# Performance work log

Hardware: AMD Instinct MI355X
Metric: run time of the kernel (lower is better)

The kernel has to match this reference:

```python
import jax, jax.numpy as jnp
import numpy as np

N, NFEAT, NHID, NHEADS = 4096, 512, 64, 8
P = 65536
ALPHA = 0.2  # LeakyReLU negative slope
NEG = -9e15  # mask value used by standard dense GAT


def setup_inputs() -> dict:
    key = jax.random.key(0)
    ks = jax.random.split(key, 9)
    x = jax.random.normal(ks[0], (N, NFEAT), dtype=jnp.float32)
    adj = (jax.random.uniform(ks[1], (N, N)) < 0.01).astype(jnp.float32)  # sparse-ish binary graph
    s = 0.05
    W_heads = jax.random.normal(ks[2], (NHEADS, NFEAT, NHID), dtype=jnp.float32) * s
    a_heads = jax.random.normal(ks[3], (NHEADS, 2 * NHID), dtype=jnp.float32) * s
    W_out = jax.random.normal(ks[4], (NHID * NHEADS, NHID), dtype=jnp.float32) * s
    a_out = jax.random.normal(ks[5], (2 * NHID,), dtype=jnp.float32) * s
    W_score = jax.random.normal(ks[6], (NHID, NHID), dtype=jnp.float32) * s
    pair1_idx = jax.random.randint(ks[7], (P,), 0, N, dtype=jnp.int32)
    pair2_idx = jax.random.randint(ks[8], (P,), 0, N, dtype=jnp.int32)
    return dict(x=x, adj=adj, W_heads=W_heads, a_heads=a_heads,
                W_out=W_out, a_out=a_out, W_score=W_score,
                pair1_idx=pair1_idx, pair2_idx=pair2_idx)


def _gat_layer(h, adj, W, a, concat):
    # Standard dense GraphAttentionLayer (no dropout: eval mode)
    Wh = h @ W                       # [N, out]
    out = W.shape[1]
    e_src = Wh @ a[:out]             # [N]
    e_dst = Wh @ a[out:]             # [N]
    e = jax.nn.leaky_relu(e_src[:, None] + e_dst[None, :], ALPHA)  # [N, N]
    logits = jnp.where(adj > 0, e, NEG)
    attn = jax.nn.softmax(logits, axis=1)
    hp = attn @ Wh                   # [N, out]
    return jax.nn.elu(hp) if concat else hp


def reference(x, adj, W_heads, a_heads, W_out, a_out, W_score, pair1_idx, pair2_idx):
    # multi-head layer, vmapped over heads; each head: [N, NHID]
    heads = jax.vmap(lambda W, a: _gat_layer(x, adj, W, a, True))(W_heads, a_heads)
    h = jnp.transpose(heads, (1, 0, 2)).reshape(N, NHEADS * NHID)  # concat dim=1
    h = jax.nn.elu(_gat_layer(h, adj, W_out, a_out, False))        # [N, NHID]
    embed1 = h[pair1_idx]            # sparse.mm(pair1_map, h) == row gather
    embed2 = h[pair2_idx]
    # diag(embed1 @ W_score @ embed2.T) == rowwise dot
    scores = jnp.sum((embed1 @ W_score) * embed2, axis=1)  # [P]
    return scores
```

## Files before the change

### kernel.cpp

```cpp
#include <hip/hip_runtime.h>
#include <math.h>

#define N 4096
#define NFEAT 512
#define NHID 64
#define NHEADS 8
#define P_PAIRS 65536
#define CAP 128
#define LRELU_ALPHA 0.2f

typedef short bf16x8 __attribute__((ext_vector_type(8)));
typedef float f32x4 __attribute__((ext_vector_type(4)));

__device__ __forceinline__ unsigned short f2bf(float f) {
  unsigned u = __float_as_uint(f);
  u = u + 0x7FFFu + ((u >> 16) & 1u);
  return (unsigned short)(u >> 16);
}
__device__ __forceinline__ float bf2f(unsigned short h) {
  return __uint_as_float(((unsigned)h) << 16);
}

__device__ __forceinline__ int swz(int row, int s) {
  int sl = ((row & 7) * 32 + s) ^ ((row & 7) << 3);
  return (row >> 3) * 256 + sl;
}

__global__ __launch_bounds__(256) void prep_all(const float* __restrict__ adj,
                                                const float* __restrict__ W1,
                                                const float* __restrict__ W2,
                                                int* __restrict__ counts,
                                                int* __restrict__ cols,
                                                unsigned short* __restrict__ w1hi,
                                                unsigned short* __restrict__ w1lo,
                                                unsigned short* __restrict__ w2hi,
                                                unsigned short* __restrict__ w2lo,
                                                float* __restrict__ sum1,
                                                float* __restrict__ sum2) {
  int b = blockIdx.x;
  if (b < N) {
    if (b == 0) {
      for (int t = threadIdx.x; t < 512; t += 256) sum1[t] = 0.f;
      if (threadIdx.x < 64) sum2[threadIdx.x] = 0.f;
    }
    __shared__ int cnt;
    if (threadIdx.x == 0) cnt = 0;
    __syncthreads();
    const float4* arow = (const float4*)(adj + (size_t)b * N);
    for (int c4 = threadIdx.x; c4 < N / 4; c4 += 256) {
      float4 v = arow[c4];
      int base = c4 * 4;
      if (v.x > 0.f) { int k = atomicAdd(&cnt, 1); if (k < CAP) cols[(size_t)b * CAP + k] = base; }
      if (v.y > 0.f) { int k = atomicAdd(&cnt, 1); if (k < CAP) cols[(size_t)b * CAP + k] = base + 1; }
      if (v.z > 0.f) { int k = atomicAdd(&cnt, 1); if (k < CAP) cols[(size_t)b * CAP + k] = base + 2; }
      if (v.w > 0.f) { int k = atomicAdd(&cnt, 1); if (k < CAP) cols[(size_t)b * CAP + k] = base + 3; }
    }
    __syncthreads();
    if (threadIdx.x == 0) counts[b] = cnt < CAP ? cnt : CAP;
  } else {
    int c = b - N;
    const float* W;
    unsigned short *hiP, *loP;
    if (c < 512) { W = W1; hiP = w1hi; loP = w1lo; }
    else         { W = W2; hiP = w2hi; loP = w2lo; c -= 512; }
    const float* Wp = W + (size_t)(c >> 6) * 512 * 64 + (c & 63);
    for (int k = threadIdx.x; k < 512; k += 256) {
      float v = Wp[(size_t)k * 64];
      unsigned short hb = f2bf(v);
      hiP[(size_t)c * 512 + k] = hb;
      loP[(size_t)c * 512 + k] = f2bf(v - bf2f(hb));
    }
  }
}

template <bool F32A>
__global__ __launch_bounds__(512) void mfma_gemm(const float* __restrict__ Af,
                                                 const unsigned short* __restrict__ Ahi,
                                                 const unsigned short* __restrict__ Alo,
                                                 const unsigned short* __restrict__ Bhi,
                                                 const unsigned short* __restrict__ Blo,
                                                 const float* __restrict__ aVec,
                                                 float* __restrict__ C,
                                                 float* __restrict__ esrc,
                                                 float* __restrict__ edst,
                                                 float* __restrict__ sumAtomic) {
  __shared__ unsigned short As[2][2][128 * 32];
  __shared__ unsigned short Bs[2][2][64 * 32];
  const int t = threadIdx.x;
  const int m0 = blockIdx.x * 128;
  const int c0 = blockIdx.y * 64;
  const int lane = t & 63, wave = t >> 6;
  const int g = lane >> 4, r = lane & 15;
  const int wm = (wave >> 1) * 32;
  const int wn = (wave & 1) * 32;
  const int sar = t >> 2, sak = (t & 3) * 8;
  const int tb = t & 255;
  const int sbr = tb >> 2, sbk = (tb & 3) * 8;
  const unsigned short* Bsel = (t < 256) ? Bhi : Blo;
  const int bhalf = (t < 256) ? 0 : 1;
  const int idxA = swz(sar, sak);
  const int idxB = swz(sbr, sbk);
  const size_t aOff = (size_t)(m0 + sar) * 512 + sak;
  const size_t bOff = (size_t)(c0 + sbr) * 512 + sbk;
  const f32x4 z = {0.f, 0.f, 0.f, 0.f};
  f32x4 acc[2][2];
  acc[0][0] = z; acc[0][1] = z; acc[1][0] = z; acc[1][1] = z;

  int4 a0, a1, b0;
  auto loadRegs = [&](int kb) {
    if constexpr (F32A) {
      float4 v0 = *(const float4*)(Af + aOff + kb);
      float4 v1 = *(const float4*)(Af + aOff + kb + 4);
      unsigned h0 = f2bf(v0.x), h1 = f2bf(v0.y), h2 = f2bf(v0.z), h3 = f2bf(v0.w);
      unsigned h4 = f2bf(v1.x), h5 = f2bf(v1.y), h6 = f2bf(v1.z), h7 = f2bf(v1.w);
      unsigned l0 = f2bf(v0.x - bf2f(h0)), l1 = f2bf(v0.y - bf2f(h1));
      unsigned l2 = f2bf(v0.z - bf2f(h2)), l3 = f2bf(v0.w - bf2f(h3));
      unsigned l4 = f2bf(v1.x - bf2f(h4)), l5 = f2bf(v1.y - bf2f(h5));
      unsigned l6 = f2bf(v1.z - bf2f(h6)), l7 = f2bf(v1.w - bf2f(h7));
      a0.x = h0 | (h1 << 16); a0.y = h2 | (h3 << 16);
      a0.z = h4 | (h5 << 16); a0.w = h6 | (h7 << 16);
      a1.x = l0 | (l1 << 16); a1.y = l2 | (l3 << 16);
      a1.z = l4 | (l5 << 16); a1.w = l6 | (l7 << 16);
    } else {
      a0 = *(const int4*)(Ahi + aOff + kb);
      a1 = *(const int4*)(Alo + aOff + kb);
    }
    b0 = *(const int4*)(Bsel + bOff + kb);
  };
  auto storeLds = [&](int buf) {
    *(int4*)(&As[buf][0][idxA]) = a0;
    *(int4*)(&As[buf][1][idxA]) = a1;
    *(int4*)(&Bs[buf][bhalf][idxB]) = b0;
  };

  loadRegs(0);
  storeLds(0);
  __syncthreads();

  for (int ch = 0; ch < 16; ++ch) {
    const int cur = ch & 1;
    if (ch < 15) loadRegs((ch + 1) * 32);
    bf16x8 ah[2], al[2], bh[2], bl[2];
#pragma unroll
    for (int f = 0; f < 2; ++f) {
      int ia = swz(wm + f * 16 + r, 8 * g);
      int ib = swz(wn + f * 16 + r, 8 * g);
      ah[f] = *(const bf16x8*)(&As[cur][0][ia]);
      al[f] = *(const bf16x8*)(&As[cur][1][ia]);
      bh[f] = *(const bf16x8*)(&Bs[cur][0][ib]);
      bl[f] = *(const bf16x8*)(&Bs[cur][1][ib]);
    }
#pragma unroll
    for (int i = 0; i < 2; ++i)
#pragma unroll
      for (int j = 0; j < 2; ++j) {
        acc[i][j] = __builtin_amdgcn_mfma_f32_16x16x32_bf16(ah[i], bh[j], acc[i][j], 0, 0, 0);
        acc[i][j] = __builtin_amdgcn_mfma_f32_16x16x32_bf16(al[i], bh[j], acc[i][j], 0, 0, 0);
        acc[i][j] = __builtin_amdgcn_mfma_f32_16x16x32_bf16(ah[i], bl[j], acc[i][j], 0, 0, 0);
      }
    if (ch < 15) {
      storeLds(cur ^ 1);
      __syncthreads();
    }
  }

  __syncthreads();
  float* Cs = (float*)&As[0][0][0];
#pragma unroll
  for (int i = 0; i < 2; ++i)
#pragma unroll
    for (int j = 0; j < 2; ++j)
#pragma unroll
      for (int q = 0; q < 4; ++q)
        Cs[(wm + i * 16 + 4 * g + q) * 64 + wn + j * 16 + r] = acc[i][j][q];
  __syncthreads();
  float* Cp = C + ((size_t)blockIdx.y * N + m0) * 64;
  const float* aV = aVec + (size_t)blockIdx.y * 128;
  float as_ = aV[lane], ad_ = aV[64 + lane];
  float cs = 0.f;
#pragma unroll
  for (int rr = 0; rr < 16; ++rr) {
    int row = wave * 16 + rr;
    float v = Cs[row * 64 + lane];
    Cp[(size_t)row * 64 + lane] = v;
    cs += v;
    float s = v * as_, d = v * ad_;
#pragma unroll
    for (int off = 32; off; off >>= 1) {
      s += __shfl_xor(s, off);
      d += __shfl_xor(d, off);
    }
    if (lane == 0) {
      esrc[(size_t)blockIdx.y * N + m0 + row] = s;
      edst[(size_t)blockIdx.y * N + m0 + row] = d;
    }
  }
  atomicAdd(&sumAtomic[blockIdx.y * 64 + lane], cs);
}

__global__ __launch_bounds__(256) void gat_attn_l1(const float* __restrict__ Wh,
                                                   const float* __restrict__ esrc,
                                                   const float* __restrict__ edst,
                                                   const int* __restrict__ counts,
                                                   const int* __restrict__ cols,
                                                   const float* __restrict__ sumWh,
                                                   unsigned short* __restrict__ hhi,
                                                   unsigned short* __restrict__ hlo) {
  int h = blockIdx.x & 7;
  int wv = threadIdx.x >> 6;
  int lane = threadIdx.x & 63;
  int sg = lane >> 4, sl = lane & 15;
  int i = (blockIdx.x >> 3) * 4 + wv;
  int cnt = counts[i];
  __shared__ int jls[4][CAP];
  __shared__ float pls[4][CAP];
  const float* WhH = Wh + (size_t)h * N * 64;
  float4 acc = {0.f, 0.f, 0.f, 0.f};
  if (cnt == 0) {
    float4 sv = *(const float4*)(sumWh + h * 64 + 4 * sl);
    acc.x = sv.x * (1.0f / N); acc.y = sv.y * (1.0f / N);
    acc.z = sv.z * (1.0f / N); acc.w = sv.w * (1.0f / N);
  } else {
    const int* cl = cols + (size_t)i * CAP;
    jls[wv][lane] = (lane < cnt) ? cl[lane] : 0;
    jls[wv][lane + 64] = (lane + 64 < cnt) ? cl[lane + 64] : 0;
    float ei = esrc[h * N + i];
    const float* ed = edst + (size_t)h * N;
    float e0 = -1e30f, e1 = -1e30f;
    if (lane < cnt) {
      float e = ei + ed[jls[wv][lane]];
      e0 = (e > 0.f) ? e : LRELU_ALPHA * e;
    }
    if (lane + 64 < cnt) {
      float e = ei + ed[jls[wv][lane + 64]];
      e1 = (e > 0.f) ? e : LRELU_ALPHA * e;
    }
    float m = fmaxf(e0, e1);
#pragma unroll
    for (int off = 32; off; off >>= 1) m = fmaxf(m, __shfl_xor(m, off));
    float p0 = (lane < cnt) ? __expf(e0 - m) : 0.f;
    float p1 = (lane + 64 < cnt) ? __expf(e1 - m) : 0.f;
    float ssum = p0 + p1;
#pragma unroll
    for (int off = 32; off; off >>= 1) ssum += __shfl_xor(ssum, off);
    pls[wv][lane] = p0;
    pls[wv][lane + 64] = p1;
    int L = (cnt + 15) & ~15;
    for (int k = 0; k < L; k += 16) {
      int j0 = jls[wv][k + sg];
      int j1 = jls[wv][k + 4 + sg];
      int j2 = jls[wv][k + 8 + sg];
      int j3 = jls[wv][k + 12 + sg];
      float4 v0 = *(const float4*)(WhH + ((size_t)j0 << 6) + 4 * sl);
      float4 v1 = *(const float4*)(WhH + ((size_t)j1 << 6) + 4 * sl);
      float4 v2 = *(const float4*)(WhH + ((size_t)j2 << 6) + 4 * sl);
      float4 v3 = *(const float4*)(WhH + ((size_t)j3 << 6) + 4 * sl);
      float q0 = pls[wv][k + sg];
      float q1 = pls[wv][k + 4 + sg];
      float q2 = pls[wv][k + 8 + sg];
      float q3 = pls[wv][k + 12 + sg];
      acc.x = fmaf(q0, v0.x, acc.x); acc.y = fmaf(q0, v0.y, acc.y);
      acc.z = fmaf(q0, v0.z, acc.z); acc.w = fmaf(q0, v0.w, acc.w);
      acc.x = fmaf(q1, v1.x, acc.x); acc.y = fmaf(q1, v1.y, acc.y);
      acc.z = fmaf(q1, v1.z, acc.z); acc.w = fmaf(q1, v1.w, acc.w);
      acc.x = fmaf(q2, v2.x, acc.x); acc.y = fmaf(q2, v2.y, acc.y);
      acc.z = fmaf(q2, v2.z, acc.z); acc.w = fmaf(q2, v2.w, acc.w);
      acc.x = fmaf(q3, v3.x, acc.x); acc.y = fmaf(q3, v3.y, acc.y);
      acc.z = fmaf(q3, v3.z, acc.z); acc.w = fmaf(q3, v3.w, acc.w);
    }
    acc.x += __shfl_xor(acc.x, 16); acc.y += __shfl_xor(acc.y, 16);
    acc.z += __shfl_xor(acc.z, 16); acc.w += __shfl_xor(acc.w, 16);
    acc.x += __shfl_xor(acc.x, 32); acc.y += __shfl_xor(acc.y, 32);
    acc.z += __shfl_xor(acc.z, 32); acc.w += __shfl_xor(acc.w, 32);
    float inv = 1.0f / ssum;
    acc.x *= inv; acc.y *= inv; acc.z *= inv; acc.w *= inv;
  }
  if (sg == 0) {
    acc.x = (acc.x > 0.f) ? acc.x : expm1f(acc.x);
    acc.y = (acc.y > 0.f) ? acc.y : expm1f(acc.y);
    acc.z = (acc.z > 0.f) ? acc.z : expm1f(acc.z);
    acc.w = (acc.w > 0.f) ? acc.w : expm1f(acc.w);
    ushort4 hi4, lo4;
    hi4.x = f2bf(acc.x); lo4.x = f2bf(acc.x - bf2f(hi4.x));
    hi4.y = f2bf(acc.y); lo4.y = f2bf(acc.y - bf2f(hi4.y));
    hi4.z = f2bf(acc.z); lo4.z = f2bf(acc.z - bf2f(hi4.z));
    hi4.w = f2bf(acc.w); lo4.w = f2bf(acc.w - bf2f(hi4.w));
    size_t o = (size_t)i * 512 + h * 64 + 4 * sl;
    *(ushort4*)(hhi + o) = hi4;
    *(ushort4*)(hlo + o) = lo4;
  }
}

__global__ __launch_bounds__(256) void gat_attn_l2(const float* __restrict__ Wh,
                                                   const float* __restrict__ esrc,
                                                   const float* __restrict__ edst,
                                                   const int* __restrict__ counts,
                                                   const int* __restrict__ cols,
                                                   const float* __restrict__ sumWh,
                                                   const float* __restrict__ Wsc,
                                                   float* __restrict__ hf,
                                                   float* __restrict__ g) {
  __shared__ float Ws[64][64];
  int t = threadIdx.x;
#pragma unroll
  for (int j = 0; j < 4; ++j) {
    int q = t + j * 256;
    int k = q >> 4, cq = (q & 15) * 4;
    *(float4*)(&Ws[k][cq]) = *(const float4*)(Wsc + k * 64 + cq);
  }
  __syncthreads();
  int wv = t >> 6;
  int lane = t & 63;
  int sg = lane >> 4, sl = lane & 15;
  int i = (blockIdx.x << 2) + wv;
  int cnt = counts[i];
  __shared__ int jls[4][CAP];
  __shared__ float pls[4][CAP];
  float v;
  if (cnt == 0) {
    v = sumWh[lane] * (1.0f / N);
  } else {
    const int* cl = cols + (size_t)i * CAP;
    jls[wv][lane] = (lane < cnt) ? cl[lane] : 0;
    jls[wv][lane + 64] = (lane + 64 < cnt) ? cl[lane + 64] : 0;
    float ei = esrc[i];
    float e0 = -1e30f, e1 = -1e30f;
    if (lane < cnt) {
      float e = ei + edst[jls[wv][lane]];
      e0 = (e > 0.f) ? e : LRELU_ALPHA * e;
    }
    if (lane + 64 < cnt) {
      float e = ei + edst[jls[wv][lane + 64]];
      e1 = (e > 0.f) ? e : LRELU_ALPHA * e;
    }
    float m = fmaxf(e0, e1);
#pragma unroll
    for (int off = 32; off; off >>= 1) m = fmaxf(m, __shfl_xor(m, off));
    float p0 = (lane < cnt) ? __expf(e0 - m) : 0.f;
    float p1 = (lane + 64 < cnt) ? __expf(e1 - m) : 0.f;
    float ssum = p0 + p1;
#pragma unroll
    for (int off = 32; off; off >>= 1) ssum += __shfl_xor(ssum, off);
    pls[wv][lane] = p0;
    pls[wv][lane + 64] = p1;
    float4 acc = {0.f, 0.f, 0.f, 0.f};
    int L = (cnt + 15) & ~15;
    for (int k = 0; k < L; k += 16) {
      int j0 = jls[wv][k + sg];
      int j1 = jls[wv][k + 4 + sg];
      int j2 = jls[wv][k + 8 + sg];
      int j3 = jls[wv][k + 12 + sg];
      float4 v0 = *(const float4*)(Wh + ((size_t)j0 << 6) + 4 * sl);
      float4 v1 = *(const float4*)(Wh + ((size_t)j1 << 6) + 4 * sl);
      float4 v2 = *(const float4*)(Wh + ((size_t)j2 << 6) + 4 * sl);
      float4 v3 = *(const float4*)(Wh + ((size_t)j3 << 6) + 4 * sl);
      float q0 = pls[wv][k + sg];
      float q1 = pls[wv][k + 4 + sg];
      float q2 = pls[wv][k + 8 + sg];
      float q3 = pls[wv][k + 12 + sg];
      acc.x = fmaf(q0, v0.x, acc.x); acc.y = fmaf(q0, v0.y, acc.y);
      acc.z = fmaf(q0, v0.z, acc.z); acc.w = fmaf(q0, v0.w, acc.w);
      acc.x = fmaf(q1, v1.x, acc.x); acc.y = fmaf(q1, v1.y, acc.y);
      acc.z = fmaf(q1, v1.z, acc.z); acc.w = fmaf(q1, v1.w, acc.w);
      acc.x = fmaf(q2, v2.x, acc.x); acc.y = fmaf(q2, v2.y, acc.y);
      acc.z = fmaf(q2, v2.z, acc.z); acc.w = fmaf(q2, v2.w, acc.w);
      acc.x = fmaf(q3, v3.x, acc.x); acc.y = fmaf(q3, v3.y, acc.y);
      acc.z = fmaf(q3, v3.z, acc.z); acc.w = fmaf(q3, v3.w, acc.w);
    }
    acc.x += __shfl_xor(acc.x, 16); acc.y += __shfl_xor(acc.y, 16);
    acc.z += __shfl_xor(acc.z, 16); acc.w += __shfl_xor(acc.w, 16);
    acc.x += __shfl_xor(acc.x, 32); acc.y += __shfl_xor(acc.y, 32);
    acc.z += __shfl_xor(acc.z, 32); acc.w += __shfl_xor(acc.w, 32);
    float cx = __shfl(acc.x, lane >> 2);
    float cy = __shfl(acc.y, lane >> 2);
    float cz = __shfl(acc.z, lane >> 2);
    float cw = __shfl(acc.w, lane >> 2);
    int cmp = lane & 3;
    v = (cmp == 0) ? cx : (cmp == 1) ? cy : (cmp == 2) ? cz : cw;
    v /= ssum;
  }
  v = (v > 0.f) ? v : expm1f(v);
  hf[((size_t)i << 6) + lane] = v;
  float gacc = 0.f;
#pragma unroll
  for (int k = 0; k < 64; ++k)
    gacc = fmaf(__shfl(v, k), Ws[k][lane], gacc);
  g[((size_t)i << 6) + lane] = gacc;
}

__global__ __launch_bounds__(256) void score_quad(const float* __restrict__ g,
                                                  const float* __restrict__ hf,
                                                  const int* __restrict__ p1,
                                                  const int* __restrict__ p2,
                                                  float* __restrict__ out) {
  int w = threadIdx.x >> 6;
  int lane = threadIdx.x & 63;
  int sub = lane >> 4, sl = lane & 15;
  int p = (((blockIdx.x << 2) + w) << 2) + sub;
  int i1 = p1[p], i2 = p2[p];
  float4 ga = *(const float4*)(g + ((size_t)i1 << 6) + sl * 4);
  float4 hb = *(const float4*)(hf + ((size_t)i2 << 6) + sl * 4);
  float v = ga.x * hb.x + ga.y * hb.y + ga.z * hb.z + ga.w * hb.w;
#pragma unroll
  for (int off = 8; off; off >>= 1) v += __shfl_xor(v, off);
  if (sl == 0) out[p] = v;
}

extern "C" void kernel_launch(void* const* d_in, const int* in_sizes, int n_in,
                              void* d_out, int out_size, void* d_ws, size_t ws_size,
                              hipStream_t stream) {
  const float* x       = (const float*)d_in[0];
  const float* adj     = (const float*)d_in[1];
  const float* W_heads = (const float*)d_in[2];
  const float* a_heads = (const float*)d_in[3];
  const float* W_out   = (const float*)d_in[4];
  const float* a_out   = (const float*)d_in[5];
  const float* W_score = (const float*)d_in[6];
  const int* p1        = (const int*)d_in[7];
  const int* p2        = (const int*)d_in[8];
  float* out           = (float*)d_out;

  char* ws = (char*)d_ws;
  size_t off = 0;
  auto alloc = [&](size_t bytes) -> void* {
    void* p = ws + off;
    off += (bytes + 255) & ~(size_t)255;
    return p;
  };
  int*   counts = (int*)alloc((size_t)N * 4);
  int*   cols   = (int*)alloc((size_t)N * CAP * 4);
  unsigned short* wt1hi = (unsigned short*)alloc((size_t)512 * 512 * 2);
  unsigned short* wt1lo = (unsigned short*)alloc((size_t)512 * 512 * 2);
  unsigned short* wt2hi = (unsigned short*)alloc((size_t)64 * 512 * 2);
  unsigned short* wt2lo = (unsigned short*)alloc((size_t)64 * 512 * 2);
  float* Wh1    = (float*)alloc((size_t)NHEADS * N * 64 * 4);
  float* es1    = (float*)alloc((size_t)NHEADS * N * 4);
  float* ed1    = (float*)alloc((size_t)NHEADS * N * 4);
  float* sum1   = (float*)alloc((size_t)512 * 4);
  unsigned short* h1hi = (unsigned short*)alloc((size_t)N * 512 * 2);
  unsigned short* h1lo = (unsigned short*)alloc((size_t)N * 512 * 2);
  float* Wh2    = (float*)alloc((size_t)N * 64 * 4);
  float* es2    = (float*)alloc((size_t)N * 4);
  float* ed2    = (float*)alloc((size_t)N * 4);
  float* sum2   = (float*)alloc((size_t)64 * 4);
  float* hf     = (float*)alloc((size_t)N * 64 * 4);
  float* g      = (float*)alloc((size_t)N * 64 * 4);

  prep_all<<<N + 576, 256, 0, stream>>>(adj, W_heads, W_out, counts, cols,
                                        wt1hi, wt1lo, wt2hi, wt2lo, sum1, sum2);

  mfma_gemm<true><<<dim3(N / 128, NHEADS), 512, 0, stream>>>(
      x, nullptr, nullptr, wt1hi, wt1lo, a_heads, Wh1, es1, ed1, sum1);

  gat_attn_l1<<<(N / 4) * NHEADS, 256, 0, stream>>>(Wh1, es1, ed1, counts, cols,
                                                    sum1, h1hi, h1lo);

  mfma_gemm<false><<<dim3(N / 128, 1), 512, 0, stream>>>(
      nullptr, h1hi, h1lo, wt2hi, wt2lo, a_out, Wh2, es2, ed2, sum2);

  gat_attn_l2<<<N / 4, 256, 0, stream>>>(Wh2, es2, ed2, counts, cols, sum2,
                                         W_score, hf, g);

  score_quad<<<P_PAIRS / 16, 256, 0, stream>>>(g, hf, p1, p2, out);
}
```

Baseline: 102.0 us.

## Fuse adjacency scan into first GEMM launch and score pass into layer-2 tail

```diff
diff --git a/kernel.cpp b/kernel.cpp
--- a/kernel.cpp
+++ b/kernel.cpp
@@ -8,6 +8,8 @@
 #define P_PAIRS 65536
 #define CAP 128
 #define LRELU_ALPHA 0.2f
+#define GEMM_BLOCKS 256
+#define TAIL_BLOCKS 512
 
 typedef short bf16x8 __attribute__((ext_vector_type(8)));
 typedef float f32x4 __attribute__((ext_vector_type(4)));
@@ -26,69 +28,44 @@
   return (row >> 3) * 256 + sl;
 }
 
-__global__ __launch_bounds__(256) void prep_all(const float* __restrict__ adj,
-                                                const float* __restrict__ W1,
-                                                const float* __restrict__ W2,
-                                                int* __restrict__ counts,
-                                                int* __restrict__ cols,
-                                                unsigned short* __restrict__ w1hi,
-                                                unsigned short* __restrict__ w1lo,
-                                                unsigned short* __restrict__ w2hi,
-                                                unsigned short* __restrict__ w2lo,
-                                                float* __restrict__ sum1,
-                                                float* __restrict__ sum2) {
-  int b = blockIdx.x;
-  if (b < N) {
-    if (b == 0) {
-      for (int t = threadIdx.x; t < 512; t += 256) sum1[t] = 0.f;
-      if (threadIdx.x < 64) sum2[threadIdx.x] = 0.f;
-    }
-    __shared__ int cnt;
-    if (threadIdx.x == 0) cnt = 0;
-    __syncthreads();
-    const float4* arow = (const float4*)(adj + (size_t)b * N);
-    for (int c4 = threadIdx.x; c4 < N / 4; c4 += 256) {
-      float4 v = arow[c4];
-      int base = c4 * 4;
-      if (v.x > 0.f) { int k = atomicAdd(&cnt, 1); if (k < CAP) cols[(size_t)b * CAP + k] = base; }
-      if (v.y > 0.f) { int k = atomicAdd(&cnt, 1); if (k < CAP) cols[(size_t)b * CAP + k] = base + 1; }
-      if (v.z > 0.f) { int k = atomicAdd(&cnt, 1); if (k < CAP) cols[(size_t)b * CAP + k] = base + 2; }
-      if (v.w > 0.f) { int k = atomicAdd(&cnt, 1); if (k < CAP) cols[(size_t)b * CAP + k] = base + 3; }
-    }
-    __syncthreads();
-    if (threadIdx.x == 0) counts[b] = cnt < CAP ? cnt : CAP;
-  } else {
-    int c = b - N;
-    const float* W;
-    unsigned short *hiP, *loP;
-    if (c < 512) { W = W1; hiP = w1hi; loP = w1lo; }
-    else         { W = W2; hiP = w2hi; loP = w2lo; c -= 512; }
-    const float* Wp = W + (size_t)(c >> 6) * 512 * 64 + (c & 63);
-    for (int k = threadIdx.x; k < 512; k += 256) {
-      float v = Wp[(size_t)k * 64];
-      unsigned short hb = f2bf(v);
-      hiP[(size_t)c * 512 + k] = hb;
-      loP[(size_t)c * 512 + k] = f2bf(v - bf2f(hb));
-    }
+__global__ __launch_bounds__(256) void prep_wt(const float* __restrict__ W1,
+                                               const float* __restrict__ W2,
+                                               unsigned short* __restrict__ w1hi,
+                                               unsigned short* __restrict__ w1lo,
+                                               unsigned short* __restrict__ w2hi,
+                                               unsigned short* __restrict__ w2lo,
+                                               int* __restrict__ barrier) {
+  if (blockIdx.x == 0 && threadIdx.x == 0) *barrier = 0;
+  int c = blockIdx.x;
+  const float* W;
+  unsigned short *hiP, *loP;
+  if (c < 512) { W = W1; hiP = w1hi; loP = w1lo; }
+  else         { W = W2; hiP = w2hi; loP = w2lo; c -= 512; }
+  const float* Wp = W + (size_t)(c >> 6) * 512 * 64 + (c & 63);
+  for (int k = threadIdx.x; k < 512; k += 256) {
+    float v = Wp[(size_t)k * 64];
+    unsigned short hb = f2bf(v);
+    hiP[(size_t)c * 512 + k] = hb;
+    loP[(size_t)c * 512 + k] = f2bf(v - bf2f(hb));
   }
 }
 
 template <bool F32A>
-__global__ __launch_bounds__(512) void mfma_gemm(const float* __restrict__ Af,
-                                                 const unsigned short* __restrict__ Ahi,
-                                                 const unsigned short* __restrict__ Alo,
-                                                 const unsigned short* __restrict__ Bhi,
-                                                 const unsigned short* __restrict__ Blo,
-                                                 const float* __restrict__ aVec,
-                                                 float* __restrict__ C,
-                                                 float* __restrict__ esrc,
-                                                 float* __restrict__ edst,
-                                                 float* __restrict__ sumAtomic) {
-  __shared__ unsigned short As[2][2][128 * 32];
-  __shared__ unsigned short Bs[2][2][64 * 32];
+__device__ __forceinline__ void gemm_body(unsigned short* As, unsigned short* Bs,
+                                          int mIdx, int head,
+                                          const float* __restrict__ Af,
+                                          const unsigned short* __restrict__ Ahi,
+                                          const unsigned short* __restrict__ Alo,
+                                          const unsigned short* __restrict__ Bhi,
+                                          const unsigned short* __restrict__ Blo,
+                                          const float* __restrict__ aVec,
+                                          float* __restrict__ C,
+                                          float* __restrict__ esrc,
+                                          float* __restrict__ edst,
+                                          float* __restrict__ cpart) {
   const int t = threadIdx.x;
-  const int m0 = blockIdx.x * 128;
-  const int c0 = blockIdx.y * 64;
+  const int m0 = mIdx * 128;
+  const int c0 = head * 64;
   const int lane = t & 63, wave = t >> 6;
   const int g = lane >> 4, r = lane & 15;
   const int wm = (wave >> 1) * 32;
@@ -128,9 +105,9 @@
     b0 = *(const int4*)(Bsel + bOff + kb);
   };
   auto storeLds = [&](int buf) {
-    *(int4*)(&As[buf][0][idxA]) = a0;
-    *(int4*)(&As[buf][1][idxA]) = a1;
-    *(int4*)(&Bs[buf][bhalf][idxB]) = b0;
+    *(int4*)(&As[(buf * 2 + 0) * 4096 + idxA]) = a0;
+    *(int4*)(&As[(buf * 2 + 1) * 4096 + idxA]) = a1;
+    *(int4*)(&Bs[(buf * 2 + bhalf) * 2048 + idxB]) = b0;
   };
 
   loadRegs(0);
@@ -145,10 +122,10 @@
     for (int f = 0; f < 2; ++f) {
       int ia = swz(wm + f * 16 + r, 8 * g);
       int ib = swz(wn + f * 16 + r, 8 * g);
-      ah[f] = *(const bf16x8*)(&As[cur][0][ia]);
-      al[f] = *(const bf16x8*)(&As[cur][1][ia]);
-      bh[f] = *(const bf16x8*)(&Bs[cur][0][ib]);
-      bl[f] = *(const bf16x8*)(&Bs[cur][1][ib]);
+      ah[f] = *(const bf16x8*)(&As[(cur * 2 + 0) * 4096 + ia]);
+      al[f] = *(const bf16x8*)(&As[(cur * 2 + 1) * 4096 + ia]);
+      bh[f] = *(const bf16x8*)(&Bs[(cur * 2 + 0) * 2048 + ib]);
+      bl[f] = *(const bf16x8*)(&Bs[(cur * 2 + 1) * 2048 + ib]);
     }
 #pragma unroll
     for (int i = 0; i < 2; ++i)
@@ -165,7 +142,7 @@
   }
 
   __syncthreads();
-  float* Cs = (float*)&As[0][0][0];
+  float* Cs = (float*)As;
 #pragma unroll
   for (int i = 0; i < 2; ++i)
 #pragma unroll
@@ -174,8 +151,8 @@
       for (int q = 0; q < 4; ++q)
         Cs[(wm + i * 16 + 4 * g + q) * 64 + wn + j * 16 + r] = acc[i][j][q];
   __syncthreads();
-  float* Cp = C + ((size_t)blockIdx.y * N + m0) * 64;
-  const float* aV = aVec + (size_t)blockIdx.y * 128;
+  float* Cp = C + ((size_t)head * N + m0) * 64;
+  const float* aV = aVec + (size_t)head * 128;
   float as_ = aV[lane], ad_ = aV[64 + lane];
   float cs = 0.f;
 #pragma unroll
@@ -191,11 +168,55 @@
       d += __shfl_xor(d, off);
     }
     if (lane == 0) {
-      esrc[(size_t)blockIdx.y * N + m0 + row] = s;
-      edst[(size_t)blockIdx.y * N + m0 + row] = d;
-    }
-  }
-  atomicAdd(&sumAtomic[blockIdx.y * 64 + lane], cs);
+      esrc[(size_t)head * N + m0 + row] = s;
+      edst[(size_t)head * N + m0 + row] = d;
+    }
+  }
+  float* red = (float*)Bs;
+  red[wave * 64 + lane] = cs;
+  __syncthreads();
+  if (wave == 0) {
+    float s = 0.f;
+#pragma unroll
+    for (int j = 0; j < 8; ++j) s += red[j * 64 + lane];
+    cpart[((size_t)head * 32 + mIdx) * 64 + lane] = s;
+  }
+}
+
+__global__ __launch_bounds__(512) void front(const float* __restrict__ x,
+                                             const float* __restrict__ adj,
+                                             const unsigned short* __restrict__ w1hi,
+                                             const unsigned short* __restrict__ w1lo,
+                                             const float* __restrict__ aVec,
+                                             float* __restrict__ Wh1,
+                                             float* __restrict__ es1,
+                                             float* __restrict__ ed1,
+                                             float* __restrict__ cpart1,
+                                             int* __restrict__ counts,
+                                             int* __restrict__ cols) {
+  __shared__ unsigned short As[2 * 2 * 4096];
+  __shared__ unsigned short Bs[2 * 2 * 2048];
+  int b = blockIdx.x;
+  if (b >= GEMM_BLOCKS) {
+    int row = b - GEMM_BLOCKS;
+    int* cntp = (int*)As;
+    if (threadIdx.x == 0) *cntp = 0;
+    __syncthreads();
+    const float4* arow = (const float4*)(adj + (size_t)row * N);
+    for (int c4 = threadIdx.x; c4 < N / 4; c4 += 512) {
+      float4 v = arow[c4];
+      int base = c4 * 4;
+      if (v.x > 0.f) { int k = atomicAdd(cntp, 1); if (k < CAP) cols[(size_t)row * CAP + k] = base; }
+      if (v.y > 0.f) { int k = atomicAdd(cntp, 1); if (k < CAP) cols[(size_t)row * CAP + k] = base + 1; }
+      if (v.z > 0.f) { int k = atomicAdd(cntp, 1); if (k < CAP) cols[(size_t)row * CAP + k] = base + 2; }
+      if (v.w > 0.f) { int k = atomicAdd(cntp, 1); if (k < CAP) cols[(size_t)row * CAP + k] = base + 3; }
+    }
+    __syncthreads();
+    if (threadIdx.x == 0) counts[row] = (*cntp < CAP) ? *cntp : CAP;
+    return;
+  }
+  gemm_body<true>(As, Bs, b & 31, b >> 5, x, nullptr, nullptr, w1hi, w1lo,
+                  aVec, Wh1, es1, ed1, cpart1);
 }
 
 __global__ __launch_bounds__(256) void gat_attn_l1(const float* __restrict__ Wh,
@@ -203,7 +224,7 @@
                                                    const float* __restrict__ edst,
                                                    const int* __restrict__ counts,
                                                    const int* __restrict__ cols,
-                                                   const float* __restrict__ sumWh,
+                                                   const float* __restrict__ cpart1,
                                                    unsigned short* __restrict__ hhi,
                                                    unsigned short* __restrict__ hlo) {
   int h = blockIdx.x & 7;
@@ -217,7 +238,11 @@
   const float* WhH = Wh + (size_t)h * N * 64;
   float4 acc = {0.f, 0.f, 0.f, 0.f};
   if (cnt == 0) {
-    float4 sv = *(const float4*)(sumWh + h * 64 + 4 * sl);
+    float4 sv = {0.f, 0.f, 0.f, 0.f};
+    for (int j = 0; j < 32; ++j) {
+      float4 p = *(const float4*)(cpart1 + ((size_t)h * 32 + j) * 64 + 4 * sl);
+      sv.x += p.x; sv.y += p.y; sv.z += p.z; sv.w += p.w;
+    }
     acc.x = sv.x * (1.0f / N); acc.y = sv.y * (1.0f / N);
     acc.z = sv.z * (1.0f / N); acc.w = sv.w * (1.0f / N);
   } else {
@@ -291,20 +316,41 @@
   }
 }
 
-__global__ __launch_bounds__(256) void gat_attn_l2(const float* __restrict__ Wh,
-                                                   const float* __restrict__ esrc,
-                                                   const float* __restrict__ edst,
-                                                   const int* __restrict__ counts,
-                                                   const int* __restrict__ cols,
-                                                   const float* __restrict__ sumWh,
-                                                   const float* __restrict__ Wsc,
-                                                   float* __restrict__ hf,
-                                                   float* __restrict__ g) {
+__global__ __launch_bounds__(512) void mid(const unsigned short* __restrict__ h1hi,
+                                           const unsigned short* __restrict__ h1lo,
+                                           const unsigned short* __restrict__ w2hi,
+                                           const unsigned short* __restrict__ w2lo,
+                                           const float* __restrict__ aVec,
+                                           float* __restrict__ Wh2,
+                                           float* __restrict__ es2,
+                                           float* __restrict__ ed2,
+                                           float* __restrict__ cpart2) {
+  __shared__ unsigned short As[2 * 2 * 4096];
+  __shared__ unsigned short Bs[2 * 2 * 2048];
+  gemm_body<false>(As, Bs, blockIdx.x, 0, nullptr, h1hi, h1lo, w2hi, w2lo,
+                   aVec, Wh2, es2, ed2, cpart2);
+}
+
+__global__ __launch_bounds__(512, 4) void tail(const float* __restrict__ Wh,
+                                               const float* __restrict__ esrc,
+                                               const float* __restrict__ edst,
+                                               const int* __restrict__ counts,
+                                               const int* __restrict__ cols,
+                                               const float* __restrict__ cpart2,
+                                               const float* __restrict__ Wsc,
+                                               const int* __restrict__ p1,
+                                               const int* __restrict__ p2,
+                                               float* __restrict__ hf,
+                                               float* __restrict__ g,
+                                               float* __restrict__ out,
+                                               int* __restrict__ barrier) {
   __shared__ float Ws[64][64];
+  __shared__ int jls[8][CAP];
+  __shared__ float pls[8][CAP];
   int t = threadIdx.x;
 #pragma unroll
-  for (int j = 0; j < 4; ++j) {
-    int q = t + j * 256;
+  for (int j = 0; j < 2; ++j) {
+    int q = t + j * 512;
     int k = q >> 4, cq = (q & 15) * 4;
     *(float4*)(&Ws[k][cq]) = *(const float4*)(Wsc + k * 64 + cq);
   }
@@ -312,13 +358,13 @@
   int wv = t >> 6;
   int lane = t & 63;
   int sg = lane >> 4, sl = lane & 15;
-  int i = (blockIdx.x << 2) + wv;
+  int i = blockIdx.x * 8 + wv;
   int cnt = counts[i];
-  __shared__ int jls[4][CAP];
-  __shared__ float pls[4][CAP];
   float v;
   if (cnt == 0) {
-    v = sumWh[lane] * (1.0f / N);
+    float s = 0.f;
+    for (int j = 0; j < 32; ++j) s += cpart2[(size_t)j * 64 + lane];
+    v = s * (1.0f / N);
   } else {
     const int* cl = cols + (size_t)i * CAP;
     jls[wv][lane] = (lane < cnt) ? cl[lane] : 0;
@@ -386,24 +432,28 @@
   for (int k = 0; k < 64; ++k)
     gacc = fmaf(__shfl(v, k), Ws[k][lane], gacc);
   g[((size_t)i << 6) + lane] = gacc;
-}
-
-__global__ __launch_bounds__(256) void score_quad(const float* __restrict__ g,
-                                                  const float* __restrict__ hf,
-                                                  const int* __restrict__ p1,
-                                                  const int* __restrict__ p2,
-                                                  float* __restrict__ out) {
-  int w = threadIdx.x >> 6;
-  int lane = threadIdx.x & 63;
-  int sub = lane >> 4, sl = lane & 15;
-  int p = (((blockIdx.x << 2) + w) << 2) + sub;
-  int i1 = p1[p], i2 = p2[p];
-  float4 ga = *(const float4*)(g + ((size_t)i1 << 6) + sl * 4);
-  float4 hb = *(const float4*)(hf + ((size_t)i2 << 6) + sl * 4);
-  float v = ga.x * hb.x + ga.y * hb.y + ga.z * hb.z + ga.w * hb.w;
-#pragma unroll
-  for (int off = 8; off; off >>= 1) v += __shfl_xor(v, off);
-  if (sl == 0) out[p] = v;
+
+  __syncthreads();
+  __threadfence();
+  if (t == 0) {
+    __hip_atomic_fetch_add(barrier, 1, __ATOMIC_ACQ_REL, __HIP_MEMORY_SCOPE_AGENT);
+    while (__hip_atomic_load(barrier, __ATOMIC_ACQUIRE, __HIP_MEMORY_SCOPE_AGENT) <
+           TAIL_BLOCKS) {}
+  }
+  __syncthreads();
+
+  int wgid = blockIdx.x * 8 + wv;
+#pragma unroll
+  for (int rep = 0; rep < 4; ++rep) {
+    int p = wgid * 16 + rep * 4 + sg;
+    int i1 = p1[p], i2 = p2[p];
+    float4 ga = *(const float4*)(g + ((size_t)i1 << 6) + sl * 4);
+    float4 hb = *(const float4*)(hf + ((size_t)i2 << 6) + sl * 4);
+    float s = ga.x * hb.x + ga.y * hb.y + ga.z * hb.z + ga.w * hb.w;
+#pragma unroll
+    for (int off = 8; off; off >>= 1) s += __shfl_xor(s, off);
+    if (sl == 0) out[p] = s;
+  }
 }
 
 extern "C" void kernel_launch(void* const* d_in, const int* in_sizes, int n_in,
@@ -436,30 +486,29 @@
   float* Wh1    = (float*)alloc((size_t)NHEADS * N * 64 * 4);
   float* es1    = (float*)alloc((size_t)NHEADS * N * 4);
   float* ed1    = (float*)alloc((size_t)NHEADS * N * 4);
-  float* sum1   = (float*)alloc((size_t)512 * 4);
+  float* cpart1 = (float*)alloc((size_t)NHEADS * 32 * 64 * 4);
   unsigned short* h1hi = (unsigned short*)alloc((size_t)N * 512 * 2);
   unsigned short* h1lo = (unsigned short*)alloc((size_t)N * 512 * 2);
   float* Wh2    = (float*)alloc((size_t)N * 64 * 4);
   float* es2    = (float*)alloc((size_t)N * 4);
   float* ed2    = (float*)alloc((size_t)N * 4);
-  float* sum2   = (float*)alloc((size_t)64 * 4);
+  float* cpart2 = (float*)alloc((size_t)32 * 64 * 4);
   float* hf     = (float*)alloc((size_t)N * 64 * 4);
   float* g      = (float*)alloc((size_t)N * 64 * 4);
-
-  prep_all<<<N + 576, 256, 0, stream>>>(adj, W_heads, W_out, counts, cols,
-                                        wt1hi, wt1lo, wt2hi, wt2lo, sum1, sum2);
-
-  mfma_gemm<true><<<dim3(N / 128, NHEADS), 512, 0, stream>>>(
-      x, nullptr, nullptr, wt1hi, wt1lo, a_heads, Wh1, es1, ed1, sum1);
+  int*   barrier = (int*)alloc(256);
+
+  prep_wt<<<576, 256, 0, stream>>>(W_heads, W_out, wt1hi, wt1lo, wt2hi, wt2lo,
+                                   barrier);
+
+  front<<<GEMM_BLOCKS + N, 512, 0, stream>>>(x, adj, wt1hi, wt1lo, a_heads,
+                                             Wh1, es1, ed1, cpart1, counts, cols);
 
   gat_attn_l1<<<(N / 4) * NHEADS, 256, 0, stream>>>(Wh1, es1, ed1, counts, cols,
-                                                    sum1, h1hi, h1lo);
-
-  mfma_gemm<false><<<dim3(N / 128, 1), 512, 0, stream>>>(
-      nullptr, h1hi, h1lo, wt2hi, wt2lo, a_out, Wh2, es2, ed2, sum2);
-
-  gat_attn_l2<<<N / 4, 256, 0, stream>>>(Wh2, es2, ed2, counts, cols, sum2,
-                                         W_score, hf, g);
-
-  score_quad<<<P_PAIRS / 16, 256, 0, stream>>>(g, hf, p1, p2, out);
-}
+                                                    cpart1, h1hi, h1lo);
+
+  mid<<<32, 512, 0, stream>>>(h1hi, h1lo, wt2hi, wt2lo, a_out, Wh2, es2, ed2,
+                              cpart2);
+
+  tail<<<TAIL_BLOCKS, 512, 0, stream>>>(Wh2, es2, ed2, counts, cols, cpart2,
+                                        W_score, p1, p2, hf, g, out, barrier);
+}
```

New measurement: 154.6 us. 1.52x slower.
